# Kernel optimization log

Measured on AMD Instinct MI355X. Metric: run time of the kernel, lower is better.

## Reference

```python
import jax, jax.numpy as jnp
import numpy as np

NEG_SLOPE = 0.01  # nn.LeakyReLU default


def preprocess_adj(A):
    # D^-1/2 A D^-1/2, expressed as row/col broadcast scaling (same math as
    # the original diag_embed + two matmuls, without the O(N^3) waste)
    d = jnp.sum(A, axis=-1)
    d_inv_sqrt = d ** -0.5
    d_inv_sqrt = jnp.where(jnp.isinf(d_inv_sqrt), 0.0, d_inv_sqrt)
    return d_inv_sqrt[..., :, None] * A * d_inv_sqrt[..., None, :]


def gcn_layer(X, A_norm, W, b, residual=False):
    H = jax.nn.leaky_relu(jnp.einsum('bnd,df->bnf', X, W) + b, NEG_SLOPE)
    out = jnp.einsum('bnm,bmf->bnf', A_norm, H)
    if residual:
        out = out + X
    return out


def setup_inputs() -> dict:
    key = jax.random.key(0)
    ks = jax.random.split(key, 8)
    B, N, D_IN, D_H, D_OUT = 8, 2048, 128, 128, 128
    scale_in = 1.0 / np.sqrt(D_IN)
    scale_h = 1.0 / np.sqrt(D_H)
    return {
        'X': jax.random.normal(ks[0], (B, N, D_IN), dtype=jnp.float32),
        'adj': jax.random.uniform(ks[1], (B, N, N), dtype=jnp.float32),
        'W1': jax.random.uniform(ks[2], (D_IN, D_H), minval=-scale_in, maxval=scale_in),
        'b1': jax.random.uniform(ks[3], (D_H,), minval=-scale_in, maxval=scale_in),
        'W2': jax.random.uniform(ks[4], (D_H, D_H), minval=-scale_h, maxval=scale_h),
        'b2': jax.random.uniform(ks[5], (D_H,), minval=-scale_h, maxval=scale_h),
        'W3': jax.random.uniform(ks[6], (D_H, D_OUT), minval=-scale_h, maxval=scale_h),
        'b3': jax.random.uniform(ks[7], (D_OUT,), minval=-scale_h, maxval=scale_h),
    }


def reference(X, adj, W1, b1, W2, b2, W3, b3):
    # Original recomputes preprocess_adj in every layer; result is identical,
    # we honor the math (compute once since adj is unchanged across layers).
    A_norm = preprocess_adj(adj)
    X = gcn_layer(X, A_norm, W1, b1, residual=False)   # GCNLayer (norm defaults False)
    X = gcn_layer(X, A_norm, W2, b2, residual=True)    # Residual_GCNLayer
    X = gcn_layer(X, A_norm, W3, b3, residual=False)   # GCNLayer
    return X
```

## Files before the change

### kernel.cpp

```cpp
#include <hip/hip_runtime.h>


typedef short bf16x8 __attribute__((ext_vector_type(8)));
typedef float f32x4 __attribute__((ext_vector_type(4)));

static __device__ __forceinline__ float bf2f(unsigned short h) {
    union { unsigned int u; float f; } v; v.u = ((unsigned int)h) << 16; return v.f;
}
static __device__ __forceinline__ unsigned short f2bf(float x) {
    union { float f; unsigned int u; } v; v.f = x;
    return (unsigned short)((v.u + 0x7FFFu + ((v.u >> 16) & 1u)) >> 16);
}

static __device__ __forceinline__ void gl2lds16(const unsigned short* g,
                                                unsigned short* l) {
    __builtin_amdgcn_global_load_lds(
        (const __attribute__((address_space(1))) unsigned int*)g,
        (__attribute__((address_space(3))) unsigned int*)l, 16, 0, 0);
}

__global__ __launch_bounds__(256) void k_pre(const float* __restrict__ adj,
                                             const float* __restrict__ W1,
                                             const float* __restrict__ W2,
                                             const float* __restrict__ W3,
                                             const float* __restrict__ b1,
                                             const float* __restrict__ b2,
                                             const float* __restrict__ b3,
                                             float* __restrict__ dinv,
                                             unsigned short* __restrict__ adjb,
                                             unsigned short* __restrict__ WT,
                                             float* __restrict__ biasf) {
    if (blockIdx.x >= 16384) {
        const int e = (blockIdx.x - 16384) * 256 + threadIdx.x;
        if (e < 49152) {
            const int w = e >> 14, r = e & 16383;
            const int f = r & 127, k = r >> 7;
            const float* W = (w == 0) ? W1 : ((w == 1) ? W2 : W3);
            WT[w * 16384 + f * 128 + k] = f2bf(W[r]);
        } else if (e < 49536) {
            const int idx = e - 49152;
            const float* bp = (idx < 128) ? b1 : ((idx < 256) ? b2 : b3);
            biasf[idx] = bp[idx & 127];
        }
        return;
    }
    const int row = blockIdx.x;
    const size_t base = (size_t)row * 2048 + threadIdx.x * 8;
    const float4 a = *(const float4*)(adj + base);
    const float4 b = *(const float4*)(adj + base + 4);
    float s = a.x + a.y + a.z + a.w + b.x + b.y + b.z + b.w;
    union { uint4 u; unsigned short h[8]; } pk;
    pk.h[0] = f2bf(a.x); pk.h[1] = f2bf(a.y); pk.h[2] = f2bf(a.z); pk.h[3] = f2bf(a.w);
    pk.h[4] = f2bf(b.x); pk.h[5] = f2bf(b.y); pk.h[6] = f2bf(b.z); pk.h[7] = f2bf(b.w);
    *(uint4*)(adjb + base) = pk.u;
#pragma unroll
    for (int off = 32; off > 0; off >>= 1) s += __shfl_down(s, off);
    __shared__ float ws[4];
    if ((threadIdx.x & 63) == 0) ws[threadIdx.x >> 6] = s;
    __syncthreads();
    if (threadIdx.x == 0) {
        float t = ws[0] + ws[1] + ws[2] + ws[3];
        dinv[row] = (t > 0.f) ? rsqrtf(t) : 0.f;
    }
}

template <int AEXT>
__global__ __launch_bounds__(256) void k_gxw(const void* __restrict__ Asrc,
                                             const unsigned short* __restrict__ WTb,
                                             const float* __restrict__ biasf,
                                             const float* __restrict__ dinv,
                                             unsigned short* __restrict__ HsT) {
    constexpr int LDK = 136;
    __shared__ unsigned short Bs[128 * LDK];

    const int tid  = threadIdx.x;
    const int wave = tid >> 6;
    const int lane = tid & 63;
    const int n_   = lane & 15;
    const int q    = lane >> 4;
    const int wm   = wave >> 1;
    const int ch   = wave & 1;

    const int r0 = blockIdx.x * 32;

#pragma unroll
    for (int it = 0; it < 8; ++it) {
        int task = tid + it * 256;
        int f  = task >> 4;
        int cj = (task & 15) * 8;
        *(uint4*)(&Bs[f * LDK + cj]) = *(const uint4*)(WTb + f * 128 + cj);
    }
    __syncthreads();

    const int arow = r0 + wm * 16 + n_;
    bf16x8 av[4];
#pragma unroll
    for (int s = 0; s < 4; ++s) {
        if (AEXT) {
            const float* p = (const float*)Asrc + (size_t)arow * 128 + s * 32 + q * 8;
            float4 uu = ((const float4*)p)[0], w = ((const float4*)p)[1];
            union { bf16x8 v; unsigned short h[8]; } r;
            r.h[0] = f2bf(uu.x); r.h[1] = f2bf(uu.y); r.h[2] = f2bf(uu.z); r.h[3] = f2bf(uu.w);
            r.h[4] = f2bf(w.x);  r.h[5] = f2bf(w.y);  r.h[6] = f2bf(w.z);  r.h[7] = f2bf(w.w);
            av[s] = r.v;
        } else {
            av[s] = *(const bf16x8*)((const unsigned short*)Asrc + (size_t)arow * 128 + s * 32 + q * 8);
        }
    }

    f32x4 acc[4];
#pragma unroll
    for (int i = 0; i < 4; ++i) acc[i] = (f32x4){0.f, 0.f, 0.f, 0.f};
#pragma unroll
    for (int s = 0; s < 4; ++s) {
#pragma unroll
        for (int nt = 0; nt < 4; ++nt) {
            bf16x8 bv = *(const bf16x8*)(&Bs[(ch * 64 + nt * 16 + n_) * LDK + s * 32 + q * 8]);
            acc[nt] = __builtin_amdgcn_mfma_f32_16x16x32_bf16(av[s], bv, acc[nt], 0, 0, 0);
        }
    }

    const int rbase = r0 + wm * 16 + q * 4;
    float dsc[4];
#pragma unroll
    for (int r = 0; r < 4; ++r) dsc[r] = dinv[rbase + r];
    const int b  = rbase >> 11;
    const int jb = rbase & 2047;
    unsigned short* Hb = HsT + (size_t)b * (128 * 2048);
#pragma unroll
    for (int nt = 0; nt < 4; ++nt) {
        const int f = ch * 64 + nt * 16 + n_;
        const float bf = biasf[f];
        unsigned short pk[4];
#pragma unroll
        for (int r = 0; r < 4; ++r) {
            float v = acc[nt][r] + bf;
            v = (v > 0.f) ? v : 0.01f * v;
            pk[r] = f2bf(v * dsc[r]);
        }
        uint2 uo;
        uo.x = (unsigned int)pk[0] | ((unsigned int)pk[1] << 16);
        uo.y = (unsigned int)pk[2] | ((unsigned int)pk[3] << 16);
        *(uint2*)(Hb + (size_t)f * 2048 + jb) = uo;
    }
}

template <int MODE, int OUT32>
__global__ __launch_bounds__(256, 2) void k_gah(const unsigned short* __restrict__ adjb,
                                                const unsigned short* __restrict__ HsT,
                                                const float* __restrict__ dinv,
                                                const unsigned short* __restrict__ resid,
                                                void* __restrict__ outp) {
    constexpr int BUFE = 10240;
    __shared__ unsigned short Sm[3 * BUFE];

    const int tid  = threadIdx.x;
    const int wave = tid >> 6;
    const int lane = tid & 63;
    const int n_   = lane & 15;
    const int q    = lane >> 4;

    const int bb = blockIdx.x;
    const int b  = bb & 7;
    const int rt = bb >> 3;
    const int row0 = b * 2048 + rt * 32;

    const unsigned short* Ag = adjb + (size_t)row0 * 2048;
    const unsigned short* Bg = HsT + (size_t)b * (128 * 2048);

    const int lr  = lane >> 3;
    const int sch = (lane & 7) ^ lr;
    const unsigned short* Asg = Ag + (size_t)(wave * 8 + lr) * 2048 + sch * 8;
    const unsigned short* Bsg0 = Bg + (size_t)(wave * 32 + 0 + lr) * 2048 + sch * 8;
    const unsigned short* Bsg1 = Bsg0 + 8 * 2048;
    const unsigned short* Bsg2 = Bsg0 + 16 * 2048;
    const unsigned short* Bsg3 = Bsg0 + 24 * 2048;
    const int dstA = wave * 512;
    const int dstB = 2048 + wave * 2048;

    const int swz = n_ & 7;
    int aoff[2][2], boff[2][2];
#pragma unroll
    for (int mi = 0; mi < 2; ++mi)
#pragma unroll
        for (int s = 0; s < 2; ++s)
            aoff[mi][s] = (n_ + mi * 16) * 64 + (((s * 4 + q) ^ swz) * 8);
#pragma unroll
    for (int nj = 0; nj < 2; ++nj)
#pragma unroll
        for (int s = 0; s < 2; ++s)
            boff[nj][s] = 2048 + (wave * 32 + nj * 16 + n_) * 64 + (((s * 4 + q) ^ swz) * 8);

    f32x4 acc[2][2];
#pragma unroll
    for (int i = 0; i < 2; ++i)
#pragma unroll
        for (int j = 0; j < 2; ++j) acc[i][j] = (f32x4){0.f, 0.f, 0.f, 0.f};

#pragma unroll
    for (int t = 0; t < 3; ++t) {
        const int kofs = t * 64;
        unsigned short* base = &Sm[t * BUFE];
        gl2lds16(Asg + kofs, base + dstA);
        gl2lds16(Bsg0 + kofs, base + dstB);
        gl2lds16(Bsg1 + kofs, base + dstB + 512);
        gl2lds16(Bsg2 + kofs, base + dstB + 1024);
        gl2lds16(Bsg3 + kofs, base + dstB + 1536);
    }

    int cur = 0;
#pragma unroll 1
    for (int t = 0; t < 32; ++t) {
        asm volatile("s_waitcnt vmcnt(10)" ::: "memory");
        __builtin_amdgcn_s_barrier();
        asm volatile("" ::: "memory");
        const unsigned short* sb = &Sm[cur * BUFE];
#pragma unroll
        for (int s = 0; s < 2; ++s) {
            bf16x8 a0 = *(const bf16x8*)(sb + aoff[0][s]);
            bf16x8 a1 = *(const bf16x8*)(sb + aoff[1][s]);
            bf16x8 b0 = *(const bf16x8*)(sb + boff[0][s]);
            bf16x8 b1 = *(const bf16x8*)(sb + boff[1][s]);
            acc[0][0] = __builtin_amdgcn_mfma_f32_16x16x32_bf16(a0, b0, acc[0][0], 0, 0, 0);
            acc[1][0] = __builtin_amdgcn_mfma_f32_16x16x32_bf16(a1, b0, acc[1][0], 0, 0, 0);
            acc[0][1] = __builtin_amdgcn_mfma_f32_16x16x32_bf16(a0, b1, acc[0][1], 0, 0, 0);
            acc[1][1] = __builtin_amdgcn_mfma_f32_16x16x32_bf16(a1, b1, acc[1][1], 0, 0, 0);
        }
        asm volatile("" ::: "memory");
        __builtin_amdgcn_s_barrier();
        asm volatile("" ::: "memory");
        {
            const int kofs = ((t + 3) & 31) * 64;
            unsigned short* base = &Sm[cur * BUFE];
            gl2lds16(Asg + kofs, base + dstA);
            gl2lds16(Bsg0 + kofs, base + dstB);
            gl2lds16(Bsg1 + kofs, base + dstB + 512);
            gl2lds16(Bsg2 + kofs, base + dstB + 1024);
            gl2lds16(Bsg3 + kofs, base + dstB + 1536);
        }
        cur = (cur == 2) ? 0 : cur + 1;
    }

    const int rb = row0 + q * 4;
    float dsc[2][4];
#pragma unroll
    for (int mi = 0; mi < 2; ++mi)
#pragma unroll
        for (int r = 0; r < 4; ++r) dsc[mi][r] = dinv[rb + mi * 16 + r];
#pragma unroll
    for (int mi = 0; mi < 2; ++mi) {
#pragma unroll
        for (int nj = 0; nj < 2; ++nj) {
            const int f = wave * 32 + nj * 16 + n_;
#pragma unroll
            for (int r = 0; r < 4; ++r) {
                const size_t gr = (size_t)(rb + mi * 16 + r);
                float v = acc[mi][nj][r] * dsc[mi][r];
                if (MODE == 2) v += bf2f(resid[gr * 128 + f]);
                if (OUT32) ((float*)outp)[gr * 128 + f] = v;
                else ((unsigned short*)outp)[gr * 128 + f] = f2bf(v);
            }
        }
    }
}

extern "C" void kernel_launch(void* const* d_in, const int* in_sizes, int n_in,
                              void* d_out, int out_size, void* d_ws, size_t ws_size,
                              hipStream_t stream) {
    const float* X   = (const float*)d_in[0];
    const float* adj = (const float*)d_in[1];
    const float* W1  = (const float*)d_in[2];
    const float* b1  = (const float*)d_in[3];
    const float* W2  = (const float*)d_in[4];
    const float* b2  = (const float*)d_in[5];
    const float* W3  = (const float*)d_in[6];
    const float* b3  = (const float*)d_in[7];

    char* ws = (char*)d_ws;
    unsigned short* adjb  = (unsigned short*)ws;
    float*          dinv  = (float*)(ws + (64u << 20));
    float*          biasf = (float*)(ws + (64u << 20) + (64u << 10));
    unsigned short* WT    = (unsigned short*)(ws + (64u << 20) + (128u << 10));
    unsigned short* HsT   = (unsigned short*)(ws + (64u << 20) + (256u << 10));
    unsigned short* Xa    = (unsigned short*)(ws + (68u << 20) + (256u << 10));
    unsigned short* X2    = (unsigned short*)(ws + (72u << 20) + (256u << 10));

    k_pre<<<16578, 256, 0, stream>>>(adj, W1, W2, W3, b1, b2, b3, dinv, adjb, WT, biasf);

    k_gxw<1><<<512, 256, 0, stream>>>(X, WT, biasf, dinv, HsT);
    k_gah<1, 0><<<512, 256, 0, stream>>>(adjb, HsT, dinv, nullptr, Xa);
    k_gxw<0><<<512, 256, 0, stream>>>(Xa, WT + 16384, biasf + 128, dinv, HsT);
    k_gah<2, 0><<<512, 256, 0, stream>>>(adjb, HsT, dinv, Xa, X2);
    k_gxw<0><<<512, 256, 0, stream>>>(X2, WT + 32768, biasf + 256, dinv, HsT);
    k_gah<1, 1><<<512, 256, 0, stream>>>(adjb, HsT, dinv, nullptr, (float*)d_out);
}
```

Baseline: 277.7 us.

## Load B operand directly into registers, keep only A tile in LDS

The aggregation kernel stops staging the H^T (B) tile through shared memory. Each lane now loads its MFMA B fragments straight from global memory into registers, using two register sets so the fragments for the next step are fetched while the current step computes. Only the adjacency (A) tile still goes through LDS, in a 4-slot ring, which shrinks LDS use from about 60KB to 16KB per block. This removes LDS write/read traffic for B and may allow more blocks per CU, at the cost of less-coalesced global loads for B and more registers per thread.

```diff
diff --git a/kernel.cpp b/kernel.cpp
--- a/kernel.cpp
+++ b/kernel.cpp
@@ -151,8 +151,8 @@
                                                 const float* __restrict__ dinv,
                                                 const unsigned short* __restrict__ resid,
                                                 void* __restrict__ outp) {
-    constexpr int BUFE = 10240;
-    __shared__ unsigned short Sm[3 * BUFE];
+    constexpr int BUFE = 2048;
+    __shared__ unsigned short Sm[4 * BUFE];
 
     const int tid  = threadIdx.x;
     const int wave = tid >> 6;
@@ -171,25 +171,18 @@
     const int lr  = lane >> 3;
     const int sch = (lane & 7) ^ lr;
     const unsigned short* Asg = Ag + (size_t)(wave * 8 + lr) * 2048 + sch * 8;
-    const unsigned short* Bsg0 = Bg + (size_t)(wave * 32 + 0 + lr) * 2048 + sch * 8;
-    const unsigned short* Bsg1 = Bsg0 + 8 * 2048;
-    const unsigned short* Bsg2 = Bsg0 + 16 * 2048;
-    const unsigned short* Bsg3 = Bsg0 + 24 * 2048;
     const int dstA = wave * 512;
-    const int dstB = 2048 + wave * 2048;
+
+    const unsigned short* Bp0 = Bg + (size_t)(wave * 32 + n_) * 2048 + q * 8;
+    const unsigned short* Bp1 = Bp0 + 16 * 2048;
 
     const int swz = n_ & 7;
-    int aoff[2][2], boff[2][2];
+    int aoff[2][2];
 #pragma unroll
     for (int mi = 0; mi < 2; ++mi)
 #pragma unroll
         for (int s = 0; s < 2; ++s)
             aoff[mi][s] = (n_ + mi * 16) * 64 + (((s * 4 + q) ^ swz) * 8);
-#pragma unroll
-    for (int nj = 0; nj < 2; ++nj)
-#pragma unroll
-        for (int s = 0; s < 2; ++s)
-            boff[nj][s] = 2048 + (wave * 32 + nj * 16 + n_) * 64 + (((s * 4 + q) ^ swz) * 8);
 
     f32x4 acc[2][2];
 #pragma unroll
@@ -197,48 +190,53 @@
 #pragma unroll
         for (int j = 0; j < 2; ++j) acc[i][j] = (f32x4){0.f, 0.f, 0.f, 0.f};
 
-#pragma unroll
-    for (int t = 0; t < 3; ++t) {
-        const int kofs = t * 64;
-        unsigned short* base = &Sm[t * BUFE];
-        gl2lds16(Asg + kofs, base + dstA);
-        gl2lds16(Bsg0 + kofs, base + dstB);
-        gl2lds16(Bsg1 + kofs, base + dstB + 512);
-        gl2lds16(Bsg2 + kofs, base + dstB + 1024);
-        gl2lds16(Bsg3 + kofs, base + dstB + 1536);
-    }
-
-    int cur = 0;
-#pragma unroll 1
-    for (int t = 0; t < 32; ++t) {
-        asm volatile("s_waitcnt vmcnt(10)" ::: "memory");
+    bf16x8 e00, e01, e10, e11, o00, o01, o10, o11;
+
+    gl2lds16(Asg, Sm + dstA);
+    e00 = *(const bf16x8*)(Bp0);
+    e01 = *(const bf16x8*)(Bp0 + 32);
+    e10 = *(const bf16x8*)(Bp1);
+    e11 = *(const bf16x8*)(Bp1 + 32);
+    gl2lds16(Asg + 64, Sm + BUFE + dstA);
+    o00 = *(const bf16x8*)(Bp0 + 64);
+    o01 = *(const bf16x8*)(Bp0 + 96);
+    o10 = *(const bf16x8*)(Bp1 + 64);
+    o11 = *(const bf16x8*)(Bp1 + 96);
+
+    auto body = [&](int tn, unsigned short* bufS, const unsigned short* bufR,
+                    bf16x8& g00, bf16x8& g01, bf16x8& g10, bf16x8& g11) {
+        const int kn = (tn & 31) * 64;
+        gl2lds16(Asg + kn, bufS + dstA);
+        asm volatile("s_waitcnt vmcnt(6)" ::: "memory");
         __builtin_amdgcn_s_barrier();
         asm volatile("" ::: "memory");
-        const unsigned short* sb = &Sm[cur * BUFE];
-#pragma unroll
-        for (int s = 0; s < 2; ++s) {
-            bf16x8 a0 = *(const bf16x8*)(sb + aoff[0][s]);
-            bf16x8 a1 = *(const bf16x8*)(sb + aoff[1][s]);
-            bf16x8 b0 = *(const bf16x8*)(sb + boff[0][s]);
-            bf16x8 b1 = *(const bf16x8*)(sb + boff[1][s]);
-            acc[0][0] = __builtin_amdgcn_mfma_f32_16x16x32_bf16(a0, b0, acc[0][0], 0, 0, 0);
-            acc[1][0] = __builtin_amdgcn_mfma_f32_16x16x32_bf16(a1, b0, acc[1][0], 0, 0, 0);
-            acc[0][1] = __builtin_amdgcn_mfma_f32_16x16x32_bf16(a0, b1, acc[0][1], 0, 0, 0);
-            acc[1][1] = __builtin_amdgcn_mfma_f32_16x16x32_bf16(a1, b1, acc[1][1], 0, 0, 0);
-        }
+        bf16x8 a00 = *(const bf16x8*)(bufR + aoff[0][0]);
+        bf16x8 a10 = *(const bf16x8*)(bufR + aoff[1][0]);
+        bf16x8 a01 = *(const bf16x8*)(bufR + aoff[0][1]);
+        bf16x8 a11 = *(const bf16x8*)(bufR + aoff[1][1]);
+        acc[0][0] = __builtin_amdgcn_mfma_f32_16x16x32_bf16(a00, g00, acc[0][0], 0, 0, 0);
+        acc[1][0] = __builtin_amdgcn_mfma_f32_16x16x32_bf16(a10, g00, acc[1][0], 0, 0, 0);
+        acc[0][1] = __builtin_amdgcn_mfma_f32_16x16x32_bf16(a00, g10, acc[0][1], 0, 0, 0);
+        acc[1][1] = __builtin_amdgcn_mfma_f32_16x16x32_bf16(a10, g10, acc[1][1], 0, 0, 0);
+        acc[0][0] = __builtin_amdgcn_mfma_f32_16x16x32_bf16(a01, g01, acc[0][0], 0, 0, 0);
+        acc[1][0] = __builtin_amdgcn_mfma_f32_16x16x32_bf16(a11, g01, acc[1][0], 0, 0, 0);
+        acc[0][1] = __builtin_amdgcn_mfma_f32_16x16x32_bf16(a01, g11, acc[0][1], 0, 0, 0);
+        acc[1][1] = __builtin_amdgcn_mfma_f32_16x16x32_bf16(a11, g11, acc[1][1], 0, 0, 0);
+        asm volatile("" ::: "memory");
+        g00 = *(const bf16x8*)(Bp0 + kn);
+        g01 = *(const bf16x8*)(Bp0 + kn + 32);
+        g10 = *(const bf16x8*)(Bp1 + kn);
+        g11 = *(const bf16x8*)(Bp1 + kn + 32);
         asm volatile("" ::: "memory");
         __builtin_amdgcn_s_barrier();
-        asm volatile("" ::: "memory");
-        {
-            const int kofs = ((t + 3) & 31) * 64;
-            unsigned short* base = &Sm[cur * BUFE];
-            gl2lds16(Asg + kofs, base + dstA);
-            gl2lds16(Bsg0 + kofs, base + dstB);
-            gl2lds16(Bsg1 + kofs, base + dstB + 512);
-            gl2lds16(Bsg2 + kofs, base + dstB + 1024);
-            gl2lds16(Bsg3 + kofs, base + dstB + 1536);
-        }
-        cur = (cur == 2) ? 0 : cur + 1;
+    };
+
+#pragma unroll 1
+    for (int kc = 0; kc < 32; kc += 4) {
+        body(kc + 2, Sm + 2 * BUFE, Sm + 0 * BUFE, e00, e01, e10, e11);
+        body(kc + 3, Sm + 3 * BUFE, Sm + 1 * BUFE, o00, o01, o10, o11);
+        body(kc + 4, Sm + 0 * BUFE, Sm + 2 * BUFE, e00, e01, e10, e11);
+        body(kc + 5, Sm + 1 * BUFE, Sm + 3 * BUFE, o00, o01, o10, o11);
     }
 
     const int rb = row0 + q * 4;
```

After: 332.2 us. 1.2x slower.
